# Kernel tuning notes

Measured on AMD Instinct MI355X. Metric: run time of the kernel, lower is better.

The kernel has to match this reference:

```python
import jax, jax.numpy as jnp
import numpy as np

B, N, M, D = 4, 2048, 2048, 512
H, HS, OUT = 8, 64, 512


def setup_inputs() -> dict:
    key = jax.random.key(0)
    ks = jax.random.split(key, 8)
    scale = 1.0 / np.sqrt(D)
    return {
        "query": jax.random.normal(ks[0], (B, N, D), jnp.float32),
        "key": jax.random.normal(ks[1], (B, M, D), jnp.float32),
        "value": jax.random.normal(ks[2], (B, M, D), jnp.float32),
        "query_kernel": jax.random.normal(ks[3], (H, D, HS), jnp.float32) * scale,
        "key_kernel": jax.random.normal(ks[4], (H, D, HS), jnp.float32) * scale,
        "value_kernel": jax.random.normal(ks[5], (H, D, HS), jnp.float32) * scale,
        "projection_kernel": jax.random.normal(ks[6], (H, HS, OUT), jnp.float32) * (1.0 / np.sqrt(H * HS)),
        "projection_bias": jnp.zeros((OUT,), jnp.float32),
    }


def reference(query, key, value, query_kernel, key_kernel, value_kernel,
              projection_kernel, projection_bias):
    # Per-head projections: B N I , H I O -> B N H O
    q = jnp.einsum('bni,hio->bnho', query, query_kernel)
    k = jnp.einsum('bmi,hio->bmho', key, key_kernel)
    v = jnp.einsum('bmi,hio->bmho', value, value_kernel)
    q = q / jnp.sqrt(jnp.asarray(HS, q.dtype))
    # Full BHNM attention matrix (matches original unfused math)
    logits = jnp.einsum('bnho,bmho->bhnm', q, k)
    attn = jax.nn.softmax(logits, axis=-1)  # dropout=0 / inference -> identity
    mh = jnp.einsum('bhnm,bmhi->bnhi', attn, v)
    out = jnp.einsum('bnhi,hio->bno', mh, projection_kernel) + projection_bias
    return out
```

## Files before the change

### kernel.cpp

```cpp
#include <hip/hip_runtime.h>
#include <hip/hip_bf16.h>


typedef __attribute__((ext_vector_type(8))) short short8;
typedef __attribute__((ext_vector_type(4))) float f32x4;

#define MFMA16(a, b, c) __builtin_amdgcn_mfma_f32_16x16x32_bf16(a, b, c, 0, 0, 0)

__device__ __forceinline__ short f2bf(float f) {
  unsigned u = __builtin_bit_cast(unsigned, f);
  u += 0x7FFF + ((u >> 16) & 1);
  return (short)(u >> 16);
}

__device__ __forceinline__ unsigned swz(unsigned byte) {
  return byte ^ (((byte >> 7) & 7) << 4);
}

__device__ __forceinline__ void gload16(const void* g, void* l) {
  __builtin_amdgcn_global_load_lds((const __attribute__((address_space(1))) void*)g,
                                   (__attribute__((address_space(3))) void*)l, 16, 0, 0);
}


__global__ void convT_qkv(const float* __restrict__ Wq, const float* __restrict__ Wk,
                          const float* __restrict__ Wv,
                          short* __restrict__ Oq, short* __restrict__ Ok,
                          short* __restrict__ Ov) {
  __shared__ short t[64][66];
  const int z = blockIdx.y;
  const float* W = (z == 0) ? Wq : (z == 1) ? Wk : Wv;
  short* O = (z == 0) ? Oq : (z == 1) ? Ok : Ov;
  const float scale = (z == 0) ? 0.125f : 1.0f;
  const int h = blockIdx.x >> 3, kb = blockIdx.x & 7;
  const int cl = threadIdx.x & 63, rw = threadIdx.x >> 6;
#pragma unroll
  for (int it = 0; it < 16; ++it) {
    int k = rw + it * 4;
    t[cl][k] = f2bf(W[((size_t)(h * 512) + kb * 64 + k) * 64 + cl] * scale);
  }
  __syncthreads();
#pragma unroll
  for (int it = 0; it < 16; ++it) {
    int hs = rw + it * 4;
    O[((size_t)(h * 64) + hs) * 512 + kb * 64 + cl] = t[hs][cl];
  }
}

__global__ void convT_p(const float* __restrict__ W, short* __restrict__ O) {
  __shared__ short t[64][66];
  const int kb = blockIdx.x & 7, nb = blockIdx.x >> 3;
  const int cl = threadIdx.x & 63, rw = threadIdx.x >> 6;
#pragma unroll
  for (int it = 0; it < 16; ++it) {
    int k = rw + it * 4;
    t[k][cl] = f2bf(W[(size_t)(kb * 64 + k) * 512 + nb * 64 + cl]);
  }
  __syncthreads();
#pragma unroll
  for (int it = 0; it < 16; ++it) {
    int n = rw + it * 4;
    O[(size_t)(nb * 64 + n) * 512 + kb * 64 + cl] = t[cl][n];
  }
}


template <int MODE, int TM>
__global__ __launch_bounds__(256, 3) void gemmT(
    const void* __restrict__ A0, const void* __restrict__ A1, const void* __restrict__ A2,
    const short* __restrict__ B0, const short* __restrict__ B1, const short* __restrict__ B2,
    void* __restrict__ O0, void* __restrict__ O1, void* __restrict__ O2,
    const float* __restrict__ bias) {
  constexpr int MT = TM / 32;
  __shared__ alignas(16) char lds[TM * 128 + 16384];
  const int z = blockIdx.z;
  const void* Ap = (z == 0) ? A0 : (z == 1) ? A1 : A2;
  const short* Bp = (z == 0) ? B0 : (z == 1) ? B1 : B2;
  void* Op = (z == 0) ? O0 : (z == 1) ? O1 : O2;

  const int tid = threadIdx.x;
  const int r0 = blockIdx.x * TM;
  const int n0 = blockIdx.y * 128;
  const int wid = tid >> 6, lane = tid & 63, g = lane >> 4, c = lane & 15;
  const int wr = wid >> 1, wc = wid & 1;
  const int rl = lane >> 3, cl = lane & 7, scol = cl ^ rl;
  const int srow = tid >> 3, sc8 = tid & 7;

  float4 fA[MT], fB[MT];

  auto LOAD_A = [&](int ks) {
    const int k0 = ks * 64;
#pragma unroll
    for (int it = 0; it < MT; ++it) {
      int row = srow + 32 * it;
      const float* src = (const float*)Ap + (size_t)(r0 + row) * 512 + k0 + sc8 * 8;
      fA[it] = *(const float4*)(src);
      fB[it] = *(const float4*)(src + 4);
    }
  };
  auto WRITE_A = [&]() {
#pragma unroll
    for (int it = 0; it < MT; ++it) {
      int row = srow + 32 * it;
      short8 s;
      s[0] = f2bf(fA[it].x); s[1] = f2bf(fA[it].y); s[2] = f2bf(fA[it].z); s[3] = f2bf(fA[it].w);
      s[4] = f2bf(fB[it].x); s[5] = f2bf(fB[it].y); s[6] = f2bf(fB[it].z); s[7] = f2bf(fB[it].w);
      *(short8*)(lds + swz(row * 128 + sc8 * 16)) = s;
    }
  };
  auto ISSUE_A = [&](int ks) {
    const int k0 = ks * 64;
#pragma unroll
    for (int i = 0; i < TM / 32; ++i) {
      int ch = wid * (TM / 32) + i;
      int row = ch * 8 + rl;
      gload16((const short*)Ap + (size_t)(r0 + row) * 512 + k0 + scol * 8, lds + ch * 1024);
    }
  };
  auto ISSUE_B = [&](int ks) {
    char* Bb = lds + TM * 128;
    const int k0 = ks * 64;
#pragma unroll
    for (int i = 0; i < 4; ++i) {
      int ch = wid * 4 + i;
      int row = ch * 8 + rl;
      gload16(Bp + (size_t)(n0 + row) * 512 + k0 + scol * 8, Bb + ch * 1024);
    }
  };

  f32x4 acc[MT][4] = {};

  if constexpr (MODE == 0) LOAD_A(0);

  for (int ks = 0; ks < 8; ++ks) {
    __syncthreads();
    if constexpr (MODE == 0) WRITE_A();
    else ISSUE_A(ks);
    ISSUE_B(ks);
    __syncthreads();
    if constexpr (MODE == 0) { if (ks < 7) LOAD_A(ks + 1); }

    const char* Bb = lds + TM * 128;
    short8 bfr[4][2];
#pragma unroll
    for (int nt = 0; nt < 4; ++nt)
#pragma unroll
      for (int kk = 0; kk < 2; ++kk) {
        int nr = wc * 64 + nt * 16 + c;
        bfr[nt][kk] = *(const short8*)(Bb + swz(nr * 128 + (g + 4 * kk) * 16));
      }
#pragma unroll
    for (int mt = 0; mt < MT; ++mt) {
      int row = wr * (TM / 2) + mt * 16 + c;
      short8 a0 = *(const short8*)(lds + swz(row * 128 + g * 16));
      short8 a1 = *(const short8*)(lds + swz(row * 128 + (g + 4) * 16));
#pragma unroll
      for (int nt = 0; nt < 4; ++nt) {
        acc[mt][nt] = MFMA16(a0, bfr[nt][0], acc[mt][nt]);
        acc[mt][nt] = MFMA16(a1, bfr[nt][1], acc[mt][nt]);
      }
    }
  }

  if constexpr (MODE == 0) {
    short* Ob = (short*)Op;
    const bool vtrans = (z == 2);
#pragma unroll
    for (int mt = 0; mt < MT; ++mt) {
      int rowb = r0 + wr * (TM / 2) + mt * 16 + g * 4;
#pragma unroll
      for (int nt = 0; nt < 4; ++nt) {
        int col = n0 + wc * 64 + nt * 16 + c;
        int hh = col >> 6, hs = col & 63;
#pragma unroll
        for (int r = 0; r < 4; ++r) {
          int row = rowb + r;
          int bb = row >> 11, nn = row & 2047;
          size_t off = vtrans ? ((((size_t)(bb * 8 + hh)) * 64 + hs) * 2048 + nn)
                              : ((((size_t)(bb * 8 + hh)) * 2048 + nn) * 64 + hs);
          Ob[off] = f2bf(acc[mt][nt][r]);
        }
      }
    }
  } else {
    float* Of = (float*)Op;
#pragma unroll
    for (int nt = 0; nt < 4; ++nt) {
      int col = n0 + wc * 64 + nt * 16 + c;
      float bv = bias[col];
#pragma unroll
      for (int mt = 0; mt < MT; ++mt) {
        int rowb = r0 + wr * (TM / 2) + mt * 16 + g * 4;
#pragma unroll
        for (int r = 0; r < 4; ++r)
          Of[(size_t)(rowb + r) * 512 + col] = acc[mt][nt][r] + bv;
      }
    }
  }
}


__global__ __launch_bounds__(256, 4) void attn64(const short* __restrict__ Qb,
                                                 const short* __restrict__ Kb,
                                                 const short* __restrict__ Vt,
                                                 short* __restrict__ MH) {
  __shared__ alignas(16) char lds[40960];
  const int flat = blockIdx.x;
  const int xcd = flat & 7, idx = flat >> 3;
  const int bh = xcd * 4 + (idx >> 5);
  const int qt = idx & 31;
  const int b = bh >> 3, h = bh & 7;

  const int tid = threadIdx.x, wid = tid >> 6, lane = tid & 63, g = lane >> 4, c = lane & 15;
  const short* Qp = Qb + ((size_t)bh * 2048 + qt * 64) * 64;
  const short* Kp = Kb + (size_t)bh * 2048 * 64;
  const short* Vp = Vt + (size_t)bh * 64 * 2048;

  const int rl = lane >> 3, cl = lane & 7, scol = cl ^ rl;

  auto ISSUE_KV = [&](int kvt, int buf) {
    char* Kd = lds + buf * 8192;
    char* Vd = lds + 16384 + buf * 8192;
#pragma unroll
    for (int i = 0; i < 2; ++i) {
      int ch = wid * 2 + i;
      int row = ch * 8 + rl;
      gload16(Kp + ((size_t)kvt * 64 + row) * 64 + scol * 8, Kd + ch * 1024);
      gload16(Vp + (size_t)row * 2048 + kvt * 64 + scol * 8, Vd + ch * 1024);
    }
  };

  short8 qf[2];
#pragma unroll
  for (int kk = 0; kk < 2; ++kk)
    qf[kk] = *(const short8*)(Qp + (wid * 16 + c) * 64 + g * 8 + kk * 32);

  f32x4 o[4] = {};
  float mrow[4], lrow[4];
#pragma unroll
  for (int r = 0; r < 4; ++r) { mrow[r] = -1e30f; lrow[r] = 0.f; }

  const int pbase = 32768 + wid * 2048;

  ISSUE_KV(0, 0);
  int cur = 0;

  for (int kvt = 0; kvt < 32; ++kvt) {
    __syncthreads();
    if (kvt < 31) ISSUE_KV(kvt + 1, cur ^ 1);
    const char* Kl = lds + cur * 8192;
    const char* Vl = lds + 16384 + cur * 8192;

    f32x4 s[4] = {};
#pragma unroll
    for (int t = 0; t < 4; ++t)
#pragma unroll
      for (int kk = 0; kk < 2; ++kk) {
        short8 kf = *(const short8*)(Kl + swz((t * 16 + c) * 128 + (g + 4 * kk) * 16));
        s[t] = MFMA16(qf[kk], kf, s[t]);
      }

#pragma unroll
    for (int r = 0; r < 4; ++r) {
      float vm = fmaxf(fmaxf(s[0][r], s[1][r]), fmaxf(s[2][r], s[3][r]));
      vm = fmaxf(vm, __shfl_xor(vm, 1));
      vm = fmaxf(vm, __shfl_xor(vm, 2));
      vm = fmaxf(vm, __shfl_xor(vm, 4));
      vm = fmaxf(vm, __shfl_xor(vm, 8));
      float mn = fmaxf(mrow[r], vm);
      float sc = __expf(mrow[r] - mn);
      float rs = 0.f;
#pragma unroll
      for (int t = 0; t < 4; ++t) {
        float p = __expf(s[t][r] - mn);
        s[t][r] = p;
        rs += p;
      }
      rs += __shfl_xor(rs, 1);
      rs += __shfl_xor(rs, 2);
      rs += __shfl_xor(rs, 4);
      rs += __shfl_xor(rs, 8);
      lrow[r] = lrow[r] * sc + rs;
      mrow[r] = mn;
#pragma unroll
      for (int t = 0; t < 4; ++t) o[t][r] *= sc;
    }

#pragma unroll
    for (int t = 0; t < 4; ++t)
#pragma unroll
      for (int r = 0; r < 4; ++r)
        *(short*)(lds + swz(pbase + (g * 4 + r) * 128 + (t * 16 + c) * 2)) = f2bf(s[t][r]);
    asm volatile("s_waitcnt lgkmcnt(0)" ::: "memory");

    short8 pa[2];
#pragma unroll
    for (int half = 0; half < 2; ++half)
      pa[half] = *(const short8*)(lds + swz(pbase + c * 128 + (g + 4 * half) * 16));
#pragma unroll
    for (int t = 0; t < 4; ++t)
#pragma unroll
      for (int half = 0; half < 2; ++half) {
        short8 vf = *(const short8*)(Vl + swz((t * 16 + c) * 128 + (g + 4 * half) * 16));
        o[t] = MFMA16(pa[half], vf, o[t]);
      }

    cur ^= 1;
  }

#pragma unroll
  for (int t = 0; t < 4; ++t)
#pragma unroll
    for (int r = 0; r < 4; ++r) {
      float val = o[t][r] / lrow[r];
      int qrow = qt * 64 + wid * 16 + g * 4 + r;
      int col = h * 64 + t * 16 + c;
      MH[((size_t)b * 2048 + qrow) * 512 + col] = f2bf(val);
    }
}


extern "C" void kernel_launch(void* const* d_in, const int* in_sizes, int n_in,
                              void* d_out, int out_size, void* d_ws, size_t ws_size,
                              hipStream_t stream) {
  const float* query = (const float*)d_in[0];
  const float* key = (const float*)d_in[1];
  const float* value = (const float*)d_in[2];
  const float* wq = (const float*)d_in[3];
  const float* wk = (const float*)d_in[4];
  const float* wv = (const float*)d_in[5];
  const float* wp = (const float*)d_in[6];
  const float* bias = (const float*)d_in[7];

  char* ws = (char*)d_ws;
  short* Wq_t = (short*)(ws + 0);
  short* Wk_t = (short*)(ws + 524288);
  short* Wv_t = (short*)(ws + 1048576);
  short* Wp_t = (short*)(ws + 1572864);
  short* Qb = (short*)(ws + 2097152);
  short* Kb = (short*)(ws + 2097152 + 8388608);
  short* Vb = (short*)(ws + 2097152 + 2 * (size_t)8388608);
  short* MH = (short*)(ws + 2097152 + 3 * (size_t)8388608);

  convT_qkv<<<dim3(64, 3), 256, 0, stream>>>(wq, wk, wv, Wq_t, Wk_t, Wv_t);
  convT_p<<<dim3(64), 256, 0, stream>>>(wp, Wp_t);
  gemmT<0, 128><<<dim3(64, 4, 3), 256, 0, stream>>>(query, key, value, Wq_t, Wk_t, Wv_t,
                                                    Qb, Kb, Vb, nullptr);
  attn64<<<dim3(1024), 256, 0, stream>>>(Qb, Kb, Vb, MH);
  gemmT<1, 64><<<dim3(128, 4, 1), 256, 0, stream>>>(MH, nullptr, nullptr, Wp_t, nullptr, nullptr,
                                                    d_out, nullptr, nullptr, bias);
}
```

Baseline: 242.9 us.

## Transpose QK^T MFMA so each lane owns one query row in softmax

Swaps the MFMA operand order so the score tile comes out transposed and each lane holds scores for a single query row. Row max and sum then reduce mostly in-register with only two cross-lane shuffles instead of four per row. It also skips the output rescale when no row max grows and packs P into 64-bit LDS stores. The cost is extra shuffles to move scale factors back to the output layout, plus a wave-divergent branch.

```diff
diff --git a/kernel.cpp b/kernel.cpp
--- a/kernel.cpp
+++ b/kernel.cpp
@@ -236,9 +236,7 @@
     qf[kk] = *(const short8*)(Qp + (wid * 16 + c) * 64 + g * 8 + kk * 32);
 
   f32x4 o[4] = {};
-  float mrow[4], lrow[4];
-#pragma unroll
-  for (int r = 0; r < 4; ++r) { mrow[r] = -1e30f; lrow[r] = 0.f; }
+  float mrow = -1e30f, lrow = 0.f;
 
   const int pbase = 32768 + wid * 2048;
 
@@ -257,40 +255,52 @@
 #pragma unroll
       for (int kk = 0; kk < 2; ++kk) {
         short8 kf = *(const short8*)(Kl + swz((t * 16 + c) * 128 + (g + 4 * kk) * 16));
-        s[t] = MFMA16(qf[kk], kf, s[t]);
-      }
-
-#pragma unroll
-    for (int r = 0; r < 4; ++r) {
-      float vm = fmaxf(fmaxf(s[0][r], s[1][r]), fmaxf(s[2][r], s[3][r]));
-      vm = fmaxf(vm, __shfl_xor(vm, 1));
-      vm = fmaxf(vm, __shfl_xor(vm, 2));
-      vm = fmaxf(vm, __shfl_xor(vm, 4));
-      vm = fmaxf(vm, __shfl_xor(vm, 8));
-      float mn = fmaxf(mrow[r], vm);
-      float sc = __expf(mrow[r] - mn);
-      float rs = 0.f;
+        s[t] = MFMA16(kf, qf[kk], s[t]);
+      }
+
+    float vm = s[0][0];
+#pragma unroll
+    for (int t = 0; t < 4; ++t)
+#pragma unroll
+      for (int r = 0; r < 4; ++r) vm = fmaxf(vm, s[t][r]);
+    vm = fmaxf(vm, __shfl_xor(vm, 16));
+    vm = fmaxf(vm, __shfl_xor(vm, 32));
+    if (__any(vm > mrow)) {
+      float mn = fmaxf(mrow, vm);
+      float sc = __expf(mrow - mn);
+      float s0 = __shfl(sc, 4 * g + 0);
+      float s1 = __shfl(sc, 4 * g + 1);
+      float s2 = __shfl(sc, 4 * g + 2);
+      float s3 = __shfl(sc, 4 * g + 3);
 #pragma unroll
       for (int t = 0; t < 4; ++t) {
-        float p = __expf(s[t][r] - mn);
+        o[t][0] *= s0; o[t][1] *= s1; o[t][2] *= s2; o[t][3] *= s3;
+      }
+      lrow *= sc;
+      mrow = mn;
+    }
+    float rs = 0.f;
+#pragma unroll
+    for (int t = 0; t < 4; ++t)
+#pragma unroll
+      for (int r = 0; r < 4; ++r) {
+        float p = __expf(s[t][r] - mrow);
         s[t][r] = p;
         rs += p;
       }
-      rs += __shfl_xor(rs, 1);
-      rs += __shfl_xor(rs, 2);
-      rs += __shfl_xor(rs, 4);
-      rs += __shfl_xor(rs, 8);
-      lrow[r] = lrow[r] * sc + rs;
-      mrow[r] = mn;
-#pragma unroll
-      for (int t = 0; t < 4; ++t) o[t][r] *= sc;
-    }
-
-#pragma unroll
-    for (int t = 0; t < 4; ++t)
-#pragma unroll
-      for (int r = 0; r < 4; ++r)
-        *(short*)(lds + swz(pbase + (g * 4 + r) * 128 + (t * 16 + c) * 2)) = f2bf(s[t][r]);
+    rs += __shfl_xor(rs, 16);
+    rs += __shfl_xor(rs, 32);
+    lrow += rs;
+
+#pragma unroll
+    for (int t = 0; t < 4; ++t) {
+      unsigned lo = (unsigned short)f2bf(s[t][0]) |
+                    ((unsigned)(unsigned short)f2bf(s[t][1]) << 16);
+      unsigned hi = (unsigned short)f2bf(s[t][2]) |
+                    ((unsigned)(unsigned short)f2bf(s[t][3]) << 16);
+      unsigned long long pw = ((unsigned long long)hi << 32) | lo;
+      *(unsigned long long*)(lds + swz(pbase + c * 128 + (16 * t + 4 * g) * 2)) = pw;
+    }
     asm volatile("s_waitcnt lgkmcnt(0)" ::: "memory");
 
     short8 pa[2];
@@ -308,15 +318,20 @@
     cur ^= 1;
   }
 
-#pragma unroll
-  for (int t = 0; t < 4; ++t)
-#pragma unroll
-    for (int r = 0; r < 4; ++r) {
-      float val = o[t][r] / lrow[r];
-      int qrow = qt * 64 + wid * 16 + g * 4 + r;
-      int col = h * 64 + t * 16 + c;
-      MH[((size_t)b * 2048 + qrow) * 512 + col] = f2bf(val);
-    }
+  float l0 = __shfl(lrow, 4 * g + 0);
+  float l1 = __shfl(lrow, 4 * g + 1);
+  float l2 = __shfl(lrow, 4 * g + 2);
+  float l3 = __shfl(lrow, 4 * g + 3);
+  float inv0 = 1.f / l0, inv1 = 1.f / l1, inv2 = 1.f / l2, inv3 = 1.f / l3;
+#pragma unroll
+  for (int t = 0; t < 4; ++t) {
+    int col = h * 64 + t * 16 + c;
+    int rowb = qt * 64 + wid * 16 + g * 4;
+    MH[((size_t)b * 2048 + rowb + 0) * 512 + col] = f2bf(o[t][0] * inv0);
+    MH[((size_t)b * 2048 + rowb + 1) * 512 + col] = f2bf(o[t][1] * inv1);
+    MH[((size_t)b * 2048 + rowb + 2) * 512 + col] = f2bf(o[t][2] * inv2);
+    MH[((size_t)b * 2048 + rowb + 3) * 512 + col] = f2bf(o[t][3] * inv3);
+  }
 }
 
 
```

After: 208.7 us. -14.1%, faster.
